# Performance work log

Hardware: AMD Instinct MI355X
Metric: run time of the kernel (lower is better)

Reference implementation:

```python
import jax, jax.numpy as jnp
import numpy as np

B, T, D, H = 128, 256, 1024, 1024


def setup_inputs() -> dict:
    key = jax.random.key(0)
    ks = jax.random.split(key, 6)
    s = 0.02
    return {
        "x": jax.random.normal(ks[0], (B, T, D), dtype=jnp.float32),
        "mask": jnp.ones((B, T), dtype=jnp.float32),
        "Wi_f": jax.random.normal(ks[1], (3 * H, D), dtype=jnp.float32) * s,
        "Wh_f": jax.random.normal(ks[2], (3 * H, H), dtype=jnp.float32) * s,
        "bi_f": jnp.zeros((3 * H,), dtype=jnp.float32),
        "bh_f": jnp.zeros((3 * H,), dtype=jnp.float32),
        "Wi_r": jax.random.normal(ks[3], (3 * H, D), dtype=jnp.float32) * s,
        "Wh_r": jax.random.normal(ks[4], (3 * H, H), dtype=jnp.float32) * s,
        "bi_r": jnp.zeros((3 * H,), dtype=jnp.float32),
        "bh_r": jnp.zeros((3 * H,), dtype=jnp.float32),
    }


def _gru_scan(x_tbd, m_tb, Wi, Wh, bi, bh):
    # x_tbd: [T,B,D], m_tb: [T,B]; returns all hidden states [T,B,H]
    h0 = jnp.zeros((x_tbd.shape[1], Wh.shape[1]), dtype=x_tbd.dtype)

    def step(h, inp):
        x_t, m_t = inp
        gi = x_t @ Wi.T + bi          # [B,3H]
        gh = h @ Wh.T + bh            # [B,3H]
        i_r, i_z, i_n = jnp.split(gi, 3, axis=-1)
        h_r, h_z, h_n = jnp.split(gh, 3, axis=-1)
        r = jax.nn.sigmoid(i_r + h_r)
        z = jax.nn.sigmoid(i_z + h_z)
        n = jnp.tanh(i_n + r * h_n)
        h_new = (1.0 - z) * n + z * h
        m = m_t[:, None]
        h_out = m * h_new + (1.0 - m) * h  # masked carry-over
        return h_out, h_out

    _, hs = jax.lax.scan(step, h0, (x_tbd, m_tb))
    return hs


def reference(x, mask, Wi_f, Wh_f, bi_f, bh_f, Wi_r, Wh_r, bi_r, bh_r):
    x_t = jnp.transpose(x, (1, 0, 2))   # [T,B,D]
    m_t = jnp.transpose(mask, (1, 0))   # [T,B]
    hs_f = _gru_scan(x_t, m_t, Wi_f, Wh_f, bi_f, bh_f)              # forward in time
    hs_r = _gru_scan(x_t[::-1], m_t[::-1], Wi_r, Wh_r, bi_r, bh_r)  # reverse in time
    hs_r = hs_r[::-1]
    out = jnp.concatenate([hs_f, hs_r], axis=-1)  # [T,B,2H]
    return jnp.transpose(out, (1, 0, 2))          # [B,T,2H]
```

## Files before the change

### kernel.cpp

```cpp
#include <hip/hip_runtime.h>
#include <hip/hip_bf16.h>

typedef __hip_bfloat16 bf16;
typedef __attribute__((ext_vector_type(8))) short bf16x8;
typedef __attribute__((ext_vector_type(4))) float f32x4;

#define GLDS16(g, l)                                                  \
  __builtin_amdgcn_global_load_lds(                                   \
      (const __attribute__((address_space(1))) void*)(g),             \
      (__attribute__((address_space(3))) void*)(l), 16, 0, 0)

__device__ __forceinline__ float bf2f(bf16 v) { return __bfloat162float(v); }
__device__ __forceinline__ short f2bf(float f) {
  bf16 b = __float2bfloat16(f);
  return *reinterpret_cast<short*>(&b);
}

__device__ __forceinline__ unsigned long long ald64(const void* p) {
  return __hip_atomic_load((const unsigned long long*)p, __ATOMIC_RELAXED,
                           __HIP_MEMORY_SCOPE_AGENT);
}
__device__ __forceinline__ void ast32(void* p, unsigned v) {
  __hip_atomic_store((unsigned*)p, v, __ATOMIC_RELAXED,
                     __HIP_MEMORY_SCOPE_AGENT);
}
__device__ __forceinline__ unsigned ald32(const void* p) {
  return __hip_atomic_load((const unsigned*)p, __ATOMIC_RELAXED,
                           __HIP_MEMORY_SCOPE_AGENT);
}

__global__ __launch_bounds__(256) void cvt_bf16(const float* __restrict__ in,
                                                bf16* __restrict__ out, int n) {
  const int i = (blockIdx.x * 256 + threadIdx.x) * 8;
  if (i >= n) return;
  const float4 u = *(const float4*)(in + i);
  const float4 v = *(const float4*)(in + i + 4);
  bf16x8 w;
  w[0] = f2bf(u.x); w[1] = f2bf(u.y); w[2] = f2bf(u.z); w[3] = f2bf(u.w);
  w[4] = f2bf(v.x); w[5] = f2bf(v.y); w[6] = f2bf(v.z); w[7] = f2bf(v.w);
  *(bf16x8*)(out + i) = w;
}

__global__ __launch_bounds__(256) void cvt_whb(const float* __restrict__ Wh_f,
                                               const float* __restrict__ Wh_r,
                                               bf16* __restrict__ Whb) {
  const int t = blockIdx.x * 256 + threadIdx.x;
  const int d = t / 393216;
  int r = t % 393216;
  const int cg = r / 6144;  r %= 6144;
  const int g = r / 2048;   r %= 2048;
  const int kk = r / 64;
  const int lane = r & 63;
  const float* Wh = d ? Wh_r : Wh_f;
  const int row = g * 1024 + cg * 16 + (lane & 15);
  const int col = kk * 32 + (lane >> 4) * 8;
  const float* s = Wh + (size_t)row * 1024 + col;
  const float4 u = *(const float4*)s;
  const float4 v = *(const float4*)(s + 4);
  bf16x8 w;
  w[0] = f2bf(u.x); w[1] = f2bf(u.y); w[2] = f2bf(u.z); w[3] = f2bf(u.w);
  w[4] = f2bf(v.x); w[5] = f2bf(v.y); w[6] = f2bf(v.z); w[7] = f2bf(v.w);
  *(bf16x8*)(Whb + (size_t)t * 8) = w;
}

__global__ __launch_bounds__(256) void gi_gemm(const bf16* __restrict__ X,
                                               const bf16* __restrict__ Wi,
                                               const float* __restrict__ bi,
                                               bf16* __restrict__ Gi) {
  __shared__ bf16 As[128 * 32];
  __shared__ bf16 Bs[128 * 32];
  const int tid = threadIdx.x;
  const int lane = tid & 63;
  const int w = tid >> 6;
  const int wm = w >> 1, wn = w & 1;
  const int m0 = blockIdx.y * 128;
  const int n0 = blockIdx.x * 128;
  const int rA = lane & 15;
  const int kl = (lane >> 4) * 8;

  f32x4 acc[4][4] = {};

  const bf16* Ab = X + (size_t)m0 * 1024;
  const bf16* Bb = Wi + (size_t)n0 * 1024;

  const int arow = tid >> 2;
  const int akk = (tid & 3) * 8;

  for (int kt = 0; kt < 1024; kt += 32) {
#pragma unroll
    for (int i = 0; i < 2; ++i) {
      GLDS16(Ab + (size_t)(i * 64 + arow) * 1024 + kt + akk,
             As + (i * 256 + w * 64) * 8);
      GLDS16(Bb + (size_t)(i * 64 + arow) * 1024 + kt + akk,
             Bs + (i * 256 + w * 64) * 8);
    }
    asm volatile("s_waitcnt vmcnt(0)" ::: "memory");
    __syncthreads();

    bf16x8 a[4], b[4];
#pragma unroll
    for (int f = 0; f < 4; ++f) {
      a[f] = *(const bf16x8*)(As + (wm * 64 + f * 16 + rA) * 32 + kl);
      b[f] = *(const bf16x8*)(Bs + (wn * 64 + f * 16 + rA) * 32 + kl);
    }
#pragma unroll
    for (int mf = 0; mf < 4; ++mf)
#pragma unroll
      for (int nf = 0; nf < 4; ++nf)
        acc[mf][nf] = __builtin_amdgcn_mfma_f32_16x16x32_bf16(
            a[mf], b[nf], acc[mf][nf], 0, 0, 0);
    __syncthreads();
  }

  const int rgrp = (lane >> 4) * 4;
#pragma unroll
  for (int nf = 0; nf < 4; ++nf) {
    const int col = n0 + wn * 64 + nf * 16 + rA;
    const float bv = bi[col];
#pragma unroll
    for (int mf = 0; mf < 4; ++mf) {
#pragma unroll
      for (int j = 0; j < 4; ++j) {
        const int row = m0 + wm * 64 + mf * 16 + rgrp + j;
        Gi[(size_t)row * 3072 + col] = __float2bfloat16(acc[mf][nf][j] + bv);
      }
    }
  }
}

__global__ __launch_bounds__(256, 1) void gru_persist_s(
    const bf16* __restrict__ Whb, const float* __restrict__ bh_f,
    const float* __restrict__ bh_r, const bf16* __restrict__ Gi,
    const float* __restrict__ mask, bf16* __restrict__ h16,
    unsigned* __restrict__ flags, float* __restrict__ out) {
  __shared__ bf16 hs[32 * 1024];
  const int tid = threadIdx.x;
  const int lane = tid & 63;
  const int w = tid >> 6;
  const int mg = w >> 1;
  const int cg = w & 1;
  const int ct = blockIdx.x;
  const int bt = blockIdx.y;
  const int dir = blockIdx.z;
  unsigned* gflags = flags + (dir * 4 + bt) * 128;

  const float* bh = dir ? bh_r : bh_f;
  const bf16* gi = Gi + (size_t)dir * (32768ull * 3072ull);
  const int bt0 = bt * 32;
  const int rA = lane & 15;
  const int klane = lane >> 4;
  const int row = mg * 16 + rA;
  const int colg = ct * 32 + cg * 16 + rA;

  bf16* hbuf0 = h16 + (size_t)(dir * 2 + 0) * 131072;
  bf16* hbuf1 = h16 + (size_t)(dir * 2 + 1) * 131072;

  const bf16* bp = Whb + (size_t)dir * 3145728 +
                   (size_t)((ct * 2 + cg) * 3) * 16384 + lane * 8;
  bf16x8 br[32], bz[32], bn[32];
#pragma unroll
  for (int kk = 0; kk < 32; ++kk) br[kk] = *(const bf16x8*)(bp + kk * 512);
#pragma unroll
  for (int kk = 0; kk < 32; ++kk)
    bz[kk] = *(const bf16x8*)(bp + 16384 + kk * 512);
#pragma unroll
  for (int kk = 0; kk < 32; ++kk)
    bn[kk] = *(const bf16x8*)(bp + 32768 + kk * 512);

  const float bhr = bh[colg];
  const float bhz = bh[1024 + colg];
  const float bhn = bh[2048 + colg];

  float hp[4] = {0.f, 0.f, 0.f, 0.f};
  const int brow0 = bt0 + mg * 16 + klane * 4;

  float gir[4], giz[4], gin[4], mk4[4];
  {
    const int time0 = dir ? 255 : 0;
#pragma unroll
    for (int j = 0; j < 4; ++j) {
      const size_t gbase = ((size_t)(brow0 + j) * 256 + time0) * 3072 + colg;
      gir[j] = bf2f(gi[gbase]);
      giz[j] = bf2f(gi[gbase + 1024]);
      gin[j] = bf2f(gi[gbase + 2048]);
      mk4[j] = mask[(brow0 + j) * 256 + time0];
    }
  }

  for (int t = 0; t < 256; ++t) {
    const int time = dir ? (255 - t) : t;
    bf16* hin = (t & 1) ? hbuf1 : hbuf0;
    bf16* hout = (t & 1) ? hbuf0 : hbuf1;

#pragma unroll
    for (int half = 0; half < 2; ++half) {
      unsigned long long vv[16];
#pragma unroll
      for (int q = 0; q < 16; ++q) {
        const int idx = (half * 16 + q) * 256 + tid;
        const int r = idx >> 8;
        const int c8 = idx & 255;
        vv[q] = ald64(hin + ((size_t)(bt0 + r) << 10) + c8 * 4);
      }
#pragma unroll
      for (int q = 0; q < 16; ++q) {
        const int idx = (half * 16 + q) * 256 + tid;
        const int r = idx >> 8;
        const int c8 = idx & 255;
        const int sw = (((c8 >> 1) ^ (r & 7)) << 4) | ((c8 & 1) << 3);
        *(unsigned long long*)((char*)hs + r * 2048 + sw) = vv[q];
      }
    }
    __syncthreads();

    f32x4 acc0 = {}, acc1 = {}, acc2 = {};
#pragma unroll
    for (int kk = 0; kk < 32; ++kk) {
      const int cidx = kk * 4 + klane;
      bf16x8 a = *(const bf16x8*)(hs + row * 1024 + ((cidx ^ (row & 7)) << 3));
      acc0 = __builtin_amdgcn_mfma_f32_16x16x32_bf16(a, br[kk], acc0, 0, 0, 0);
      acc1 = __builtin_amdgcn_mfma_f32_16x16x32_bf16(a, bz[kk], acc1, 0, 0, 0);
      acc2 = __builtin_amdgcn_mfma_f32_16x16x32_bf16(a, bn[kk], acc2, 0, 0, 0);
    }

    float hnv[4];
#pragma unroll
    for (int j = 0; j < 4; ++j) {
      const float gr = acc0[j] + bhr + gir[j];
      const float gz = acc1[j] + bhz + giz[j];
      const float ghn = acc2[j] + bhn;
      const float r = 1.f / (1.f + __expf(-gr));
      const float z = 1.f / (1.f + __expf(-gz));
      const float nin = gin[j] + r * ghn;
      const float n = 1.f - 2.f / (__expf(2.f * nin) + 1.f);
      float hn = (1.f - z) * n + z * hp[j];
      hn = mk4[j] * hn + (1.f - mk4[j]) * hp[j];
      hp[j] = hn;
      hnv[j] = hn;
      const unsigned short hb = (unsigned short)f2bf(hn);
      const unsigned nb = (unsigned)__shfl_xor((int)hb, 1);
      if (!(lane & 1))
        ast32(hout + (((size_t)brow0 + j) << 10) + colg,
              (unsigned)hb | (nb << 16));
    }

    asm volatile("s_waitcnt vmcnt(0)" ::: "memory");
    __syncthreads();
    if (tid == 0) ast32(&gflags[ct], (unsigned)(t + 1));

#pragma unroll
    for (int j = 0; j < 4; ++j)
      out[(((size_t)(brow0 + j)) * 256 + time) * 2048 + (size_t)(dir * 1024) +
          colg] = hnv[j];

    if (t < 255) {
      const int tn = dir ? (254 - t) : (t + 1);
#pragma unroll
      for (int j = 0; j < 4; ++j) {
        const size_t gbase = ((size_t)(brow0 + j) * 256 + tn) * 3072 + colg;
        gir[j] = bf2f(gi[gbase]);
        giz[j] = bf2f(gi[gbase + 1024]);
        gin[j] = bf2f(gi[gbase + 2048]);
        mk4[j] = mask[(brow0 + j) * 256 + tn];
      }
      if (w == 0) {
        unsigned v;
        do {
          __builtin_amdgcn_s_sleep(1);
          v = ald32(&gflags[lane & 31]);
        } while (__any((int)(v < (unsigned)(t + 1))));
      }
      __builtin_amdgcn_sched_barrier(0);
      __syncthreads();
    }
  }
}

extern "C" void kernel_launch(void* const* d_in, const int* in_sizes, int n_in,
                              void* d_out, int out_size, void* d_ws,
                              size_t ws_size, hipStream_t stream) {
  const float* x = (const float*)d_in[0];
  const float* mask = (const float*)d_in[1];
  const float* Wi_f = (const float*)d_in[2];
  const float* Wh_f = (const float*)d_in[3];
  const float* bi_f = (const float*)d_in[4];
  const float* bh_f = (const float*)d_in[5];
  const float* Wi_r = (const float*)d_in[6];
  const float* Wh_r = (const float*)d_in[7];
  const float* bi_r = (const float*)d_in[8];
  const float* bh_r = (const float*)d_in[9];
  float* out = (float*)d_out;

  char* ws = (char*)d_ws;
  const size_t GI_ELEMS = 32768ull * 3072ull;
  bf16* Gi = (bf16*)ws;
  bf16* Whb = (bf16*)(ws + 2 * GI_ELEMS * sizeof(bf16));
  bf16* h16 = Whb + 2 * 3145728;
  unsigned* flags = (unsigned*)((char*)h16 + 1048576);

  bf16* Xb = (bf16*)d_out;
  bf16* Wib_f = Xb + 33554432;
  bf16* Wib_r = Wib_f + 3145728;

  hipMemsetAsync(h16, 0, 1048576 + 4096, stream);

  cvt_bf16<<<16384, 256, 0, stream>>>(x, Xb, 33554432);
  cvt_bf16<<<1536, 256, 0, stream>>>(Wi_f, Wib_f, 3145728);
  cvt_bf16<<<1536, 256, 0, stream>>>(Wi_r, Wib_r, 3145728);
  cvt_whb<<<3072, 256, 0, stream>>>(Wh_f, Wh_r, Whb);

  gi_gemm<<<dim3(24, 256), 256, 0, stream>>>(Xb, Wib_f, bi_f, Gi);
  gi_gemm<<<dim3(24, 256), 256, 0, stream>>>(Xb, Wib_r, bi_r, Gi + GI_ELEMS);

  gru_persist_s<<<dim3(32, 4, 2), 256, 0, stream>>>(Whb, bh_f, bh_r, Gi, mask,
                                                    h16, flags, out);
}
```

Before: 2.469 ms.

## Halve persistent GRU grid, widen column tiles, stream Wh from global each step

The persistent recurrent kernel now launches 16 column tiles per batch tile instead of 32. Each wave handles 16 columns across all 32 batch rows, and the LDS A-fragments are reused across two MFMA row groups. The Wh tile is no longer held in registers for the whole run; it is reloaded from global or L2 on every timestep, and the flag barrier spins over 16 blocks instead of 32. This cuts the number of blocks that synchronise per step and halves the redundant h staging into LDS. The cost is reading 3 MB of recurrent weights per direction from cache every step, where they used to stay in registers.

```diff
diff --git a/kernel.cpp b/kernel.cpp
--- a/kernel.cpp
+++ b/kernel.cpp
@@ -128,7 +128,7 @@
   }
 }
 
-__global__ __launch_bounds__(256, 1) void gru_persist_s(
+__global__ __launch_bounds__(256, 1) void gru_persist_w(
     const bf16* __restrict__ Whb, const float* __restrict__ bh_f,
     const float* __restrict__ bh_r, const bf16* __restrict__ Gi,
     const float* __restrict__ mask, bf16* __restrict__ h16,
@@ -137,8 +137,6 @@
   const int tid = threadIdx.x;
   const int lane = tid & 63;
   const int w = tid >> 6;
-  const int mg = w >> 1;
-  const int cg = w & 1;
   const int ct = blockIdx.x;
   const int bt = blockIdx.y;
   const int dir = blockIdx.z;
@@ -149,42 +147,35 @@
   const int bt0 = bt * 32;
   const int rA = lane & 15;
   const int klane = lane >> 4;
-  const int row = mg * 16 + rA;
-  const int colg = ct * 32 + cg * 16 + rA;
+  const int colg = ct * 64 + w * 16 + rA;
 
   bf16* hbuf0 = h16 + (size_t)(dir * 2 + 0) * 131072;
   bf16* hbuf1 = h16 + (size_t)(dir * 2 + 1) * 131072;
 
   const bf16* bp = Whb + (size_t)dir * 3145728 +
-                   (size_t)((ct * 2 + cg) * 3) * 16384 + lane * 8;
-  bf16x8 br[32], bz[32], bn[32];
-#pragma unroll
-  for (int kk = 0; kk < 32; ++kk) br[kk] = *(const bf16x8*)(bp + kk * 512);
-#pragma unroll
-  for (int kk = 0; kk < 32; ++kk)
-    bz[kk] = *(const bf16x8*)(bp + 16384 + kk * 512);
-#pragma unroll
-  for (int kk = 0; kk < 32; ++kk)
-    bn[kk] = *(const bf16x8*)(bp + 32768 + kk * 512);
+                   (size_t)((ct * 4 + w) * 3) * 16384 + lane * 8;
 
   const float bhr = bh[colg];
   const float bhz = bh[1024 + colg];
   const float bhn = bh[2048 + colg];
 
-  float hp[4] = {0.f, 0.f, 0.f, 0.f};
-  const int brow0 = bt0 + mg * 16 + klane * 4;
-
-  float gir[4], giz[4], gin[4], mk4[4];
+  float hp[2][4] = {};
+  const int brow0 = bt0 + klane * 4;
+
+  float gir[2][4], giz[2][4], gin[2][4], mk4[2][4];
   {
     const int time0 = dir ? 255 : 0;
 #pragma unroll
-    for (int j = 0; j < 4; ++j) {
-      const size_t gbase = ((size_t)(brow0 + j) * 256 + time0) * 3072 + colg;
-      gir[j] = bf2f(gi[gbase]);
-      giz[j] = bf2f(gi[gbase + 1024]);
-      gin[j] = bf2f(gi[gbase + 2048]);
-      mk4[j] = mask[(brow0 + j) * 256 + time0];
-    }
+    for (int m = 0; m < 2; ++m)
+#pragma unroll
+      for (int j = 0; j < 4; ++j) {
+        const int brow = brow0 + m * 16 + j;
+        const size_t gbase = ((size_t)brow * 256 + time0) * 3072 + colg;
+        gir[m][j] = bf2f(gi[gbase]);
+        giz[m][j] = bf2f(gi[gbase + 1024]);
+        gin[m][j] = bf2f(gi[gbase + 2048]);
+        mk4[m][j] = mask[brow * 256 + time0];
+      }
   }
 
   for (int t = 0; t < 256; ++t) {
@@ -213,61 +204,76 @@
     }
     __syncthreads();
 
-    f32x4 acc0 = {}, acc1 = {}, acc2 = {};
+    f32x4 acc[3][2] = {};
 #pragma unroll
     for (int kk = 0; kk < 32; ++kk) {
       const int cidx = kk * 4 + klane;
-      bf16x8 a = *(const bf16x8*)(hs + row * 1024 + ((cidx ^ (row & 7)) << 3));
-      acc0 = __builtin_amdgcn_mfma_f32_16x16x32_bf16(a, br[kk], acc0, 0, 0, 0);
-      acc1 = __builtin_amdgcn_mfma_f32_16x16x32_bf16(a, bz[kk], acc1, 0, 0, 0);
-      acc2 = __builtin_amdgcn_mfma_f32_16x16x32_bf16(a, bn[kk], acc2, 0, 0, 0);
-    }
-
-    float hnv[4];
-#pragma unroll
-    for (int j = 0; j < 4; ++j) {
-      const float gr = acc0[j] + bhr + gir[j];
-      const float gz = acc1[j] + bhz + giz[j];
-      const float ghn = acc2[j] + bhn;
-      const float r = 1.f / (1.f + __expf(-gr));
-      const float z = 1.f / (1.f + __expf(-gz));
-      const float nin = gin[j] + r * ghn;
-      const float n = 1.f - 2.f / (__expf(2.f * nin) + 1.f);
-      float hn = (1.f - z) * n + z * hp[j];
-      hn = mk4[j] * hn + (1.f - mk4[j]) * hp[j];
-      hp[j] = hn;
-      hnv[j] = hn;
-      const unsigned short hb = (unsigned short)f2bf(hn);
-      const unsigned nb = (unsigned)__shfl_xor((int)hb, 1);
-      if (!(lane & 1))
-        ast32(hout + (((size_t)brow0 + j) << 10) + colg,
-              (unsigned)hb | (nb << 16));
-    }
+      const int r1 = 16 + rA;
+      bf16x8 a0 = *(const bf16x8*)(hs + rA * 1024 + ((cidx ^ (rA & 7)) << 3));
+      bf16x8 a1 = *(const bf16x8*)(hs + r1 * 1024 + ((cidx ^ (r1 & 7)) << 3));
+      bf16x8 b0 = *(const bf16x8*)(bp + kk * 512);
+      bf16x8 b1 = *(const bf16x8*)(bp + 16384 + kk * 512);
+      bf16x8 b2 = *(const bf16x8*)(bp + 32768 + kk * 512);
+      acc[0][0] = __builtin_amdgcn_mfma_f32_16x16x32_bf16(a0, b0, acc[0][0], 0, 0, 0);
+      acc[0][1] = __builtin_amdgcn_mfma_f32_16x16x32_bf16(a1, b0, acc[0][1], 0, 0, 0);
+      acc[1][0] = __builtin_amdgcn_mfma_f32_16x16x32_bf16(a0, b1, acc[1][0], 0, 0, 0);
+      acc[1][1] = __builtin_amdgcn_mfma_f32_16x16x32_bf16(a1, b1, acc[1][1], 0, 0, 0);
+      acc[2][0] = __builtin_amdgcn_mfma_f32_16x16x32_bf16(a0, b2, acc[2][0], 0, 0, 0);
+      acc[2][1] = __builtin_amdgcn_mfma_f32_16x16x32_bf16(a1, b2, acc[2][1], 0, 0, 0);
+    }
+
+    float hnv[2][4];
+#pragma unroll
+    for (int m = 0; m < 2; ++m)
+#pragma unroll
+      for (int j = 0; j < 4; ++j) {
+        const float gr = acc[0][m][j] + bhr + gir[m][j];
+        const float gz = acc[1][m][j] + bhz + giz[m][j];
+        const float ghn = acc[2][m][j] + bhn;
+        const float r = 1.f / (1.f + __expf(-gr));
+        const float z = 1.f / (1.f + __expf(-gz));
+        const float nin = gin[m][j] + r * ghn;
+        const float n = 1.f - 2.f / (__expf(2.f * nin) + 1.f);
+        float hn = (1.f - z) * n + z * hp[m][j];
+        hn = mk4[m][j] * hn + (1.f - mk4[m][j]) * hp[m][j];
+        hp[m][j] = hn;
+        hnv[m][j] = hn;
+        const unsigned short hb = (unsigned short)f2bf(hn);
+        const unsigned nb = (unsigned)__shfl_xor((int)hb, 1);
+        if (!(lane & 1))
+          ast32(hout + (((size_t)brow0 + m * 16 + j) << 10) + colg,
+                (unsigned)hb | (nb << 16));
+      }
 
     asm volatile("s_waitcnt vmcnt(0)" ::: "memory");
     __syncthreads();
     if (tid == 0) ast32(&gflags[ct], (unsigned)(t + 1));
 
 #pragma unroll
-    for (int j = 0; j < 4; ++j)
-      out[(((size_t)(brow0 + j)) * 256 + time) * 2048 + (size_t)(dir * 1024) +
-          colg] = hnv[j];
+    for (int m = 0; m < 2; ++m)
+#pragma unroll
+      for (int j = 0; j < 4; ++j)
+        out[(((size_t)(brow0 + m * 16 + j)) * 256 + time) * 2048 +
+            (size_t)(dir * 1024) + colg] = hnv[m][j];
 
     if (t < 255) {
       const int tn = dir ? (254 - t) : (t + 1);
 #pragma unroll
-      for (int j = 0; j < 4; ++j) {
-        const size_t gbase = ((size_t)(brow0 + j) * 256 + tn) * 3072 + colg;
-        gir[j] = bf2f(gi[gbase]);
-        giz[j] = bf2f(gi[gbase + 1024]);
-        gin[j] = bf2f(gi[gbase + 2048]);
-        mk4[j] = mask[(brow0 + j) * 256 + tn];
-      }
+      for (int m = 0; m < 2; ++m)
+#pragma unroll
+        for (int j = 0; j < 4; ++j) {
+          const int brow = brow0 + m * 16 + j;
+          const size_t gbase = ((size_t)brow * 256 + tn) * 3072 + colg;
+          gir[m][j] = bf2f(gi[gbase]);
+          giz[m][j] = bf2f(gi[gbase + 1024]);
+          gin[m][j] = bf2f(gi[gbase + 2048]);
+          mk4[m][j] = mask[brow * 256 + tn];
+        }
       if (w == 0) {
         unsigned v;
         do {
           __builtin_amdgcn_s_sleep(1);
-          v = ald32(&gflags[lane & 31]);
+          v = ald32(&gflags[lane & 15]);
         } while (__any((int)(v < (unsigned)(t + 1))));
       }
       __builtin_amdgcn_sched_barrier(0);
@@ -312,6 +318,6 @@
   gi_gemm<<<dim3(24, 256), 256, 0, stream>>>(Xb, Wib_f, bi_f, Gi);
   gi_gemm<<<dim3(24, 256), 256, 0, stream>>>(Xb, Wib_r, bi_r, Gi + GI_ELEMS);
 
-  gru_persist_s<<<dim3(32, 4, 2), 256, 0, stream>>>(Whb, bh_f, bh_r, Gi, mask,
+  gru_persist_w<<<dim3(16, 4, 2), 256, 0, stream>>>(Whb, bh_f, bh_r, Gi, mask,
                                                     h16, flags, out);
 }
```

After: 4.785 ms. 1.94x slower.
